# Kernel optimization log

Measured on AMD Instinct MI355X. Metric: run time of the kernel, lower is better.

## Reference

```python
import jax, jax.numpy as jnp
import numpy as np

N, C, H, DH = 4096, 256, 8, 32
E = 32768
MAX_SPD = 3
DEG_B = 8
LN_EPS = 1e-5


def _ln(h, g, b):
    mu = jnp.mean(h, axis=-1, keepdims=True)
    var = jnp.mean((h - mu) ** 2, axis=-1, keepdims=True)
    return g * (h - mu) / jnp.sqrt(var + LN_EPS) + b


def setup_inputs() -> dict:
    key = jax.random.key(0)
    ks = jax.random.split(key, 16)
    s = 1.0 / np.sqrt(C).astype(np.float32)
    s4 = 1.0 / np.sqrt(4 * C).astype(np.float32)
    return {
        "x": jax.random.normal(ks[0], (N, C), jnp.float32),
        "edge_index": jax.random.randint(ks[1], (2, E), 0, N, dtype=jnp.int32),
        "Wq": jax.random.normal(ks[2], (C, C), jnp.float32) * s,
        "bq": jnp.zeros((C,), jnp.float32),
        "Wk": jax.random.normal(ks[3], (C, C), jnp.float32) * s,
        "bk": jnp.zeros((C,), jnp.float32),
        "Wv": jax.random.normal(ks[4], (C, C), jnp.float32) * s,
        "bv": jnp.zeros((C,), jnp.float32),
        "Wo": jax.random.normal(ks[5], (C, C), jnp.float32) * s,
        "bo": jnp.zeros((C,), jnp.float32),
        "W1": jax.random.normal(ks[6], (C, 4 * C), jnp.float32) * s,
        "b1": jnp.zeros((4 * C,), jnp.float32),
        "W2": jax.random.normal(ks[7], (4 * C, C), jnp.float32) * s4,
        "b2": jnp.zeros((C,), jnp.float32),
        "g1": jnp.ones((C,), jnp.float32),
        "beta1": jnp.zeros((C,), jnp.float32),
        "g2": jnp.ones((C,), jnp.float32),
        "beta2": jnp.zeros((C,), jnp.float32),
        # spd_emb is zero-init in torch; use small random so the bias path is exercised
        "spd_emb": jax.random.normal(ks[8], (MAX_SPD + 2, H), jnp.float32) * 0.02,
        "in_deg_emb": jax.random.normal(ks[9], (DEG_B + 1, C), jnp.float32) * 0.02,
        "out_deg_emb": jax.random.normal(ks[10], (DEG_B + 1, C), jnp.float32) * 0.02,
        "et_bias": jax.random.normal(ks[11], (), jnp.float32) * 0.02,
    }


def _bucket(d):
    # floor(log2(d+1)) clamped to [0, DEG_B]
    return jnp.clip(jnp.floor(jnp.log2(d + 1.0)), 0, DEG_B).astype(jnp.int32)


def _spd_buckets(src, dst):
    # use_reverse_spd=True: adjacency A[row=dst, col=src]; anchors = dst, probe = src.
    # Frontier F starts as identity over all nodes (superset of unique-anchor columns;
    # extra columns never probed -> identical result to torch's unique-anchor version).
    F = jnp.eye(N, dtype=jnp.float32)
    spd = jnp.full((E,), MAX_SPD + 1, dtype=jnp.int32)
    unset = jnp.ones((E,), dtype=bool)
    for k in range(1, MAX_SPD + 1):
        # (A @ F) > 0  via edge-gather + per-row max (binary reachability)
        F = (jax.ops.segment_max(F[src], dst, num_segments=N) > 0).astype(jnp.float32)
        reach = F[src, dst] > 0  # probe anchor column dst at row src
        newly = unset & reach
        spd = jnp.where(newly, k, spd)
        unset = unset & ~newly
    return jnp.clip(spd, 1, MAX_SPD + 1)


def reference(x, edge_index, Wq, bq, Wk, bk, Wv, bv, Wo, bo, W1, b1, W2, b2,
              g1, beta1, g2, beta2, spd_emb, in_deg_emb, out_deg_emb, et_bias):
    src, dst = edge_index[0], edge_index[1]
    ones = jnp.ones((E,), jnp.float32)
    in_deg = jax.ops.segment_sum(ones, dst, num_segments=N)
    out_deg = jax.ops.segment_sum(ones, src, num_segments=N)
    x_in = x + in_deg_emb[_bucket(in_deg)] + out_deg_emb[_bucket(out_deg)]

    spd = _spd_buckets(src, dst)  # [E] int in [1, MAX_SPD+1]

    xn = _ln(x_in, g1, beta1)
    Q = (xn @ Wq + bq).reshape(N, H, DH)
    K = (xn @ Wk + bk).reshape(N, H, DH)
    V = (xn @ Wv + bv).reshape(N, H, DH)

    scores = jnp.sum(Q[dst] * K[src], axis=-1) / np.sqrt(DH)  # [E, H]
    scores = scores + spd_emb[spd] + et_bias

    # segment softmax over edges sharing a destination node
    m = jax.ops.segment_max(scores, dst, num_segments=N)  # [N, H]
    m = jnp.where(jnp.isfinite(m), m, 0.0)
    e = jnp.exp(scores - m[dst])
    ssum = jax.ops.segment_sum(e, dst, num_segments=N)
    w = e / jnp.where(ssum[dst] > 0, ssum[dst], 1.0)  # [E, H]

    msg = jax.ops.segment_sum(w[:, :, None] * V[src], dst, num_segments=N)  # [N,H,DH]
    h = x_in + msg.reshape(N, C) @ Wo + bo
    hn = _ln(h, g2, beta2)
    ff = jax.nn.gelu(hn @ W1 + b1, approximate=False) @ W2 + b2
    return h + ff
```

## Files before the change

kernel.cpp:

```cpp
#include <hip/hip_runtime.h>
#include <math.h>

#define NN 4096
#define CC 256
#define HH 8
#define DHD 32
#define EE 32768
#define FW 128
#define MAXD 128

typedef float f32x4 __attribute__((ext_vector_type(4)));
typedef __bf16 bf16x8 __attribute__((ext_vector_type(8)));
typedef __bf16 bf16x4 __attribute__((ext_vector_type(4)));

__device__ __forceinline__ int bucketf(int d){
  float l = log2f((float)d + 1.0f);
  int b = (int)floorf(l);
  return b < 0 ? 0 : (b > 8 ? 8 : b);
}

__global__ void k_deg(const int* __restrict__ src, const int* __restrict__ dst,
                      int* __restrict__ indeg, int* __restrict__ outdeg){
  int e = blockIdx.x*256 + threadIdx.x;
  if(e < EE){
    atomicAdd(&indeg[dst[e]], 1);
    atomicAdd(&outdeg[src[e]], 1);
  }
}

__global__ void k_scan(const int* __restrict__ deg, int* __restrict__ offs){
  __shared__ int part[1024];
  int t = threadIdx.x;
  int v0=deg[t*4], v1=deg[t*4+1], v2=deg[t*4+2], v3=deg[t*4+3];
  int s = v0+v1+v2+v3;
  part[t] = s;
  __syncthreads();
  for(int d=1; d<1024; d<<=1){
    int x = (t>=d) ? part[t-d] : 0;
    __syncthreads();
    part[t] += x;
    __syncthreads();
  }
  int base = (t>0) ? part[t-1] : 0;
  offs[t*4]   = base;
  offs[t*4+1] = base+v0;
  offs[t*4+2] = base+v0+v1;
  offs[t*4+3] = base+v0+v1+v2;
  if(t==1023) offs[4096] = base+s;
}

__global__ void k_scatter(const int* __restrict__ src, const int* __restrict__ dst,
                          const int* __restrict__ offs, int* __restrict__ cursor,
                          int* __restrict__ nsrc){
  int e = blockIdx.x*256+threadIdx.x;
  if(e<EE){
    int d = dst[e], s = src[e];
    int p = atomicAdd(&cursor[d],1);
    nsrc[offs[d]+p] = s;
  }
}

__global__ void k_mid(const int* __restrict__ offs, const int* __restrict__ nsrc,
                      unsigned* __restrict__ F1,
                      const float* __restrict__ x, const int* __restrict__ indeg,
                      const int* __restrict__ outdeg, const float* __restrict__ iemb,
                      const float* __restrict__ oemb, const float* __restrict__ g,
                      const float* __restrict__ be, float* __restrict__ x_in,
                      __bf16* __restrict__ xn){
  int b = blockIdx.x;
  int tid = threadIdx.x;
  if(b < 2048){
    int d = b*2 + (tid>>7);
    int w = tid & 127;
    int o0 = offs[d], o1 = offs[d+1];
    unsigned v = 0;
    for(int i=o0;i<o1;i++){
      int s = nsrc[i];
      if((s>>5) == w) v |= 1u << (s&31);
    }
    F1[(size_t)d*FW + w] = v;
    return;
  }
  int node = (b-2048)*4 + (tid >> 6);
  int lane = tid & 63;
  int bi = bucketf(indeg[node]);
  int bo = bucketf(outdeg[node]);
  float4 xv = ((const float4*)(x + (size_t)node*CC))[lane];
  float4 iv = ((const float4*)(iemb + (size_t)bi*CC))[lane];
  float4 ov = ((const float4*)(oemb + (size_t)bo*CC))[lane];
  float4 v;
  v.x = xv.x+iv.x+ov.x; v.y = xv.y+iv.y+ov.y;
  v.z = xv.z+iv.z+ov.z; v.w = xv.w+iv.w+ov.w;
  ((float4*)(x_in + (size_t)node*CC))[lane] = v;
  float s  = v.x+v.y+v.z+v.w;
  float sq = v.x*v.x+v.y*v.y+v.z*v.z+v.w*v.w;
  #pragma unroll
  for(int m=32;m>=1;m>>=1){ s += __shfl_xor(s,m); sq += __shfl_xor(sq,m); }
  float mu  = s * (1.0f/CC);
  float var = sq * (1.0f/CC) - mu*mu;
  float inv = rsqrtf(var + 1e-5f);
  float4 gv = ((const float4*)g)[lane];
  float4 bv = ((const float4*)be)[lane];
  bf16x4 o;
  o[0] = (__bf16)(gv.x*(v.x-mu)*inv + bv.x);
  o[1] = (__bf16)(gv.y*(v.y-mu)*inv + bv.y);
  o[2] = (__bf16)(gv.z*(v.z-mu)*inv + bv.z);
  o[3] = (__bf16)(gv.w*(v.w-mu)*inv + bv.w);
  *(bf16x4*)(xn + (size_t)node*CC + lane*4) = o;
}

__global__ void k_prop(const int* __restrict__ offs, const int* __restrict__ nsrc,
                       const unsigned* __restrict__ Fin, unsigned* __restrict__ Fout){
  int d = blockIdx.x; int w = threadIdx.x;
  int o0 = offs[d], o1 = offs[d+1];
  unsigned v = 0;
  for(int i=o0;i<o1;i++){
    int s = nsrc[i];
    v |= Fin[(size_t)s*FW + w];
  }
  Fout[(size_t)d*FW + w] = v;
}

__global__ void k_ln(const float* __restrict__ in, const float* __restrict__ g,
                     const float* __restrict__ b, __bf16* __restrict__ out){
  int node = blockIdx.x*4 + (threadIdx.x >> 6);
  int lane = threadIdx.x & 63;
  float4 v = ((const float4*)(in + (size_t)node*CC))[lane];
  float s  = v.x+v.y+v.z+v.w;
  float sq = v.x*v.x+v.y*v.y+v.z*v.z+v.w*v.w;
  #pragma unroll
  for(int m=32;m>=1;m>>=1){ s += __shfl_xor(s,m); sq += __shfl_xor(sq,m); }
  float mu  = s * (1.0f/CC);
  float var = sq * (1.0f/CC) - mu*mu;
  float inv = rsqrtf(var + 1e-5f);
  float4 gv = ((const float4*)g)[lane];
  float4 bv = ((const float4*)b)[lane];
  bf16x4 o;
  o[0] = (__bf16)(gv.x*(v.x-mu)*inv + bv.x);
  o[1] = (__bf16)(gv.y*(v.y-mu)*inv + bv.y);
  o[2] = (__bf16)(gv.z*(v.z-mu)*inv + bv.z);
  o[3] = (__bf16)(gv.w*(v.w-mu)*inv + bv.w);
  *(bf16x4*)(out + (size_t)node*CC + lane*4) = o;
}

__global__ void k_pre(const float* __restrict__ Wq, const float* __restrict__ Wk,
                      const float* __restrict__ Wv, const float* __restrict__ Wo,
                      const float* __restrict__ W1, const float* __restrict__ W2,
                      const float* __restrict__ bq, const float* __restrict__ bk,
                      const float* __restrict__ bv,
                      __bf16* __restrict__ WqkvT, __bf16* __restrict__ WoT,
                      __bf16* __restrict__ W1T, __bf16* __restrict__ W2T,
                      float* __restrict__ bqkv, int* __restrict__ zero_base){
  int b = blockIdx.x;
  int tid = threadIdx.x;
  if(b >= 193){
    zero_base[(b-193)*256 + tid] = 0;
    return;
  }
  if(b == 192){
    bqkv[tid]     = bq[tid];
    bqkv[256+tid] = bk[tid];
    bqkv[512+tid] = bv[tid];
    return;
  }
  const float* W; __bf16* Wt; int K, N, tile;
  if(b < 16)      { W=Wq; Wt=WqkvT;        K=256;  N=256;  tile=b; }
  else if(b < 32) { W=Wk; Wt=WqkvT+65536;  K=256;  N=256;  tile=b-16; }
  else if(b < 48) { W=Wv; Wt=WqkvT+131072; K=256;  N=256;  tile=b-32; }
  else if(b < 64) { W=Wo; Wt=WoT;          K=256;  N=256;  tile=b-48; }
  else if(b < 128){ W=W1; Wt=W1T;          K=256;  N=1024; tile=b-64; }
  else            { W=W2; Wt=W2T;          K=1024; N=256;  tile=b-128; }
  int nK = K/64;
  int tk = tile % nK, tn = tile / nK;
  __shared__ float T[64][65];
  int c = tid & 63, r0 = tid >> 6;
  #pragma unroll
  for(int i=0;i<16;i++){
    int row = r0*16 + i;
    T[row][c] = W[(size_t)(tk*64+row)*N + tn*64 + c];
  }
  __syncthreads();
  #pragma unroll
  for(int i=0;i<16;i++){
    int row = r0*16 + i;
    Wt[(size_t)(tn*64+row)*K + tk*64 + c] = (__bf16)T[c][row];
  }
}

template<int MODE>
__global__ __launch_bounds__(256) void k_bgemm(const __bf16* __restrict__ A, const __bf16* __restrict__ Bt,
                       const float* __restrict__ bias, const float* __restrict__ add,
                       float* __restrict__ outf, __bf16* __restrict__ outb,
                       int M, int N, int K){
  __shared__ __bf16 As[64*64];
  __shared__ __bf16 Bs[64*64];
  const int tid = threadIdx.x;
  const int lane = tid & 63, w = tid >> 6;
  const int wr = w >> 1, wc = w & 1;
  const int l15 = lane & 15, g = lane >> 4;
  const int bm = blockIdx.y*64, bn = blockIdx.x*64;
  f32x4 acc[2][2] = {};
  for(int k0=0; k0<K; k0+=64){
    #pragma unroll
    for(int rep=0; rep<2; rep++){
      int q = tid + rep*256;
      int row = q>>3;
      int scb = ((q&7)*16) ^ ((row&7)<<4);
      const __bf16* srcA = A  + (size_t)(bm+row)*K + k0 + (scb>>1);
      const __bf16* srcB = Bt + (size_t)(bn+row)*K + k0 + (scb>>1);
      __builtin_amdgcn_global_load_lds(
        (const __attribute__((address_space(1))) void*)srcA,
        (__attribute__((address_space(3))) void*)((char*)As + q*16), 16, 0, 0);
      __builtin_amdgcn_global_load_lds(
        (const __attribute__((address_space(1))) void*)srcB,
        (__attribute__((address_space(3))) void*)((char*)Bs + q*16), 16, 0, 0);
    }
    __syncthreads();
    #pragma unroll
    for(int ks=0; ks<2; ks++){
      bf16x8 a[2], b[2];
      #pragma unroll
      for(int i=0;i<2;i++){
        int row = wr*32 + i*16 + l15;
        int byte_ = row*128 + ks*64 + g*16; byte_ ^= (row&7)<<4;
        a[i] = *(const bf16x8*)((const char*)As + byte_);
      }
      #pragma unroll
      for(int j=0;j<2;j++){
        int row = wc*32 + j*16 + l15;
        int byte_ = row*128 + ks*64 + g*16; byte_ ^= (row&7)<<4;
        b[j] = *(const bf16x8*)((const char*)Bs + byte_);
      }
      #pragma unroll
      for(int i=0;i<2;i++)
        #pragma unroll
        for(int j=0;j<2;j++)
          acc[i][j] = __builtin_amdgcn_mfma_f32_16x16x32_bf16(a[i], b[j], acc[i][j], 0, 0, 0);
    }
    __syncthreads();
  }
  #pragma unroll
  for(int i=0;i<2;i++){
    #pragma unroll
    for(int j=0;j<2;j++){
      int col = bn + wc*32 + j*16 + l15;
      float bv = bias[col];
      #pragma unroll
      for(int r=0;r<4;r++){
        int rowg = bm + wr*32 + i*16 + g*4 + r;
        float v = acc[i][j][r] + bv;
        if(MODE==1) v += add[(size_t)rowg*N + col];
        if(MODE==2){
          v = 0.5f*v*(1.0f + erff(v*0.70710678118654752f));
          outb[(size_t)rowg*N + col] = (__bf16)v;
        } else if(MODE==3){
          outb[(size_t)rowg*N + col] = (__bf16)v;
        } else {
          outf[(size_t)rowg*N + col] = v;
        }
      }
    }
  }
}

__global__ void k_sagg(const int* __restrict__ nsrc, const int* __restrict__ offs,
                       const __bf16* __restrict__ QKV,
                       const unsigned* __restrict__ F1, const unsigned* __restrict__ F2,
                       const unsigned* __restrict__ F3,
                       const float* __restrict__ spde, __bf16* __restrict__ msg){
  __shared__ float scs[MAXD][9];
  __shared__ int   sl[MAXD];
  __shared__ int   spi[MAXD];
  const int d = blockIdx.x;
  const int t = threadIdx.x;
  const int o0 = offs[d];
  int deg = offs[d+1] - o0; if(deg > MAXD) deg = MAXD;
  if(t < deg){
    int s = nsrc[o0+t];
    sl[t] = s;
    size_t wi = (size_t)s*FW + (d>>5); unsigned bb = 1u << (d&31);
    int sp = 4;
    if(F3[wi] & bb) sp = 3;
    if(F2[wi] & bb) sp = 2;
    if(F1[wi] & bb) sp = 1;
    spi[t] = sp;
  }
  __syncthreads();
  { const int h = t & 7, i0 = t >> 3;
    const bf16x8* qr = (const bf16x8*)(QKV + (size_t)d*768 + h*DHD);
    for(int i=i0; i<deg; i+=32){
      const bf16x8* kr = (const bf16x8*)(QKV + (size_t)sl[i]*768 + 256 + h*DHD);
      float acc = 0.f;
      #pragma unroll
      for(int j=0;j<4;j++){
        bf16x8 kv = kr[j], qv = qr[j];
        #pragma unroll
        for(int u=0;u<8;u++) acc += (float)qv[u] * (float)kv[u];
      }
      scs[i][h] = acc * 0.17677669529663687f + spde[spi[i]*HH + h];
    }
  }
  __syncthreads();
  { const int h = t >> 5, l = t & 31;
    float m = -3.0e38f;
    for(int i=l;i<deg;i+=32) m = fmaxf(m, scs[i][h]);
    #pragma unroll
    for(int mk=16;mk>=1;mk>>=1) m = fmaxf(m, __shfl_xor(m,mk));
    float ss = 0.f;
    for(int i=l;i<deg;i+=32) ss += expf(scs[i][h]-m);
    #pragma unroll
    for(int mk=16;mk>=1;mk>>=1) ss += __shfl_xor(ss,mk);
    float inv = (ss>0.f) ? 1.f/ss : 1.f;
    for(int i=l;i<deg;i+=32) scs[i][h] = expf(scs[i][h]-m)*inv;
  }
  __syncthreads();
  { const int h = t >> 5, c = t & 31;
    float acc = 0.f;
    for(int i=0;i<deg;i++)
      acc += scs[i][h] * (float)QKV[(size_t)sl[i]*768 + 512 + h*DHD + c];
    msg[(size_t)d*CC + h*DHD + c] = (__bf16)acc;
  }
}

extern "C" void kernel_launch(void* const* d_in, const int* in_sizes, int n_in,
                              void* d_out, int out_size, void* d_ws, size_t ws_size,
                              hipStream_t stream){
  const float* x  = (const float*)d_in[0];
  const int*  ei  = (const int*)d_in[1];
  const float* Wq = (const float*)d_in[2];  const float* bq = (const float*)d_in[3];
  const float* Wk = (const float*)d_in[4];  const float* bk = (const float*)d_in[5];
  const float* Wv = (const float*)d_in[6];  const float* bv = (const float*)d_in[7];
  const float* Wo = (const float*)d_in[8];  const float* bo = (const float*)d_in[9];
  const float* W1 = (const float*)d_in[10]; const float* b1 = (const float*)d_in[11];
  const float* W2 = (const float*)d_in[12]; const float* b2 = (const float*)d_in[13];
  const float* g1 = (const float*)d_in[14]; const float* be1= (const float*)d_in[15];
  const float* g2 = (const float*)d_in[16]; const float* be2= (const float*)d_in[17];
  const float* spde = (const float*)d_in[18];
  const float* iemb = (const float*)d_in[19];
  const float* oemb = (const float*)d_in[20];
  const float* etb  = (const float*)d_in[21]; (void)etb;
  const int* src = ei;
  const int* dst = ei + EE;
  float* out = (float*)d_out;

  const size_t NC = (size_t)NN*CC;
  float* ws   = (float*)d_ws;
  float* x_in = ws;
  float* hbuf = ws + NC;
  int* indeg  = (int*)(ws + 2*NC);
  int* outdeg = indeg + NN;
  int* cursor = outdeg + NN;
  unsigned* F1 = (unsigned*)(cursor + NN);
  unsigned* F2 = F1 + (size_t)NN*FW;
  unsigned* F3 = F2 + (size_t)NN*FW;
  __bf16* QKV  = (__bf16*)(F3 + (size_t)NN*FW);
  __bf16* xn_bf  = (__bf16*)(ws + 5517312);
  __bf16* msg_bf = (__bf16*)(ws + 6041600);
  __bf16* WqkvT  = (__bf16*)(ws + 6565888);
  __bf16* WoT    = WqkvT + 196608;
  __bf16* W1T    = WoT + 65536;
  __bf16* W2T    = W1T + 262144;
  float* bqkv    = ws + 6959104;
  int* offs      = (int*)(bqkv + 768);
  int* nsrc      = offs + NN + 4;
  __bf16* ff1_bf = (__bf16*)(ws + 2*NC);
  __bf16* hn_bf  = (__bf16*)(ws + 4*NC);

  k_pre<<<241,256,0,stream>>>(Wq,Wk,Wv,Wo,W1,W2,bq,bk,bv,WqkvT,WoT,W1T,W2T,bqkv,indeg);
  k_deg<<<EE/256,256,0,stream>>>(src,dst,indeg,outdeg);
  k_scan<<<1,1024,0,stream>>>(indeg,offs);
  k_scatter<<<EE/256,256,0,stream>>>(src,dst,offs,cursor,nsrc);
  k_mid<<<3072,256,0,stream>>>(offs,nsrc,F1,x,indeg,outdeg,iemb,oemb,g1,be1,x_in,xn_bf);
  k_prop<<<NN,FW,0,stream>>>(offs,nsrc,F1,F2);
  k_prop<<<NN,FW,0,stream>>>(offs,nsrc,F2,F3);

  dim3 gq(768/64, NN/64);
  k_bgemm<3><<<gq,256,0,stream>>>(xn_bf, WqkvT, bqkv, nullptr, nullptr, QKV, NN, 768, 256);

  k_sagg<<<NN,256,0,stream>>>(nsrc,offs,QKV,F1,F2,F3,spde,msg_bf);

  dim3 go(256/64, NN/64);
  k_bgemm<1><<<go,256,0,stream>>>(msg_bf, WoT, bo, x_in, hbuf, nullptr, NN, 256, 256);
  k_ln <<<NN/4,256,0,stream>>>(hbuf,g2,be2,hn_bf);
  dim3 gf1(1024/64, NN/64);
  k_bgemm<2><<<gf1,256,0,stream>>>(hn_bf, W1T, b1, nullptr, nullptr, ff1_bf, NN, 1024, 256);
  dim3 gf2(256/64, NN/64);
  k_bgemm<1><<<gf2,256,0,stream>>>(ff1_bf, W2T, b2, hbuf, out, nullptr, NN, 256, 1024);
}
```

Before: 92.04 us.

## Replace CSR build with fixed-width adjacency and fuse third hop with QKV GEMM

Drops the degree-count and prefix-scan kernels by scattering sources straight into a fixed-stride per-node slot array (MAXD=64), with the atomic cursor reused as in-degree and out-degree counted in the scatter. The third frontier propagation is merged into the QKV projection GEMM as one launch with block-index branching, so the two independent jobs share the GPU. This cuts launches and serial single-block scan work. It truncates neighbors beyond 64 per node, which is only safe if no node exceeds that in-degree (MAXD was also lowered from 128 for the aggregation).

```diff
diff --git a/kernel.cpp b/kernel.cpp
--- a/kernel.cpp
+++ b/kernel.cpp
@@ -7,7 +7,7 @@
 #define DHD 32
 #define EE 32768
 #define FW 128
-#define MAXD 128
+#define MAXD 64
 
 typedef float f32x4 __attribute__((ext_vector_type(4)));
 typedef __bf16 bf16x8 __attribute__((ext_vector_type(8)));
@@ -19,50 +19,21 @@
   return b < 0 ? 0 : (b > 8 ? 8 : b);
 }
 
-__global__ void k_deg(const int* __restrict__ src, const int* __restrict__ dst,
-                      int* __restrict__ indeg, int* __restrict__ outdeg){
-  int e = blockIdx.x*256 + threadIdx.x;
-  if(e < EE){
-    atomicAdd(&indeg[dst[e]], 1);
-    atomicAdd(&outdeg[src[e]], 1);
-  }
-}
-
-__global__ void k_scan(const int* __restrict__ deg, int* __restrict__ offs){
-  __shared__ int part[1024];
-  int t = threadIdx.x;
-  int v0=deg[t*4], v1=deg[t*4+1], v2=deg[t*4+2], v3=deg[t*4+3];
-  int s = v0+v1+v2+v3;
-  part[t] = s;
-  __syncthreads();
-  for(int d=1; d<1024; d<<=1){
-    int x = (t>=d) ? part[t-d] : 0;
-    __syncthreads();
-    part[t] += x;
-    __syncthreads();
-  }
-  int base = (t>0) ? part[t-1] : 0;
-  offs[t*4]   = base;
-  offs[t*4+1] = base+v0;
-  offs[t*4+2] = base+v0+v1;
-  offs[t*4+3] = base+v0+v1+v2;
-  if(t==1023) offs[4096] = base+s;
-}
-
 __global__ void k_scatter(const int* __restrict__ src, const int* __restrict__ dst,
-                          const int* __restrict__ offs, int* __restrict__ cursor,
+                          int* __restrict__ cursor, int* __restrict__ outdeg,
                           int* __restrict__ nsrc){
   int e = blockIdx.x*256+threadIdx.x;
   if(e<EE){
     int d = dst[e], s = src[e];
+    atomicAdd(&outdeg[s],1);
     int p = atomicAdd(&cursor[d],1);
-    nsrc[offs[d]+p] = s;
-  }
-}
-
-__global__ void k_mid(const int* __restrict__ offs, const int* __restrict__ nsrc,
+    if(p < MAXD) nsrc[d*MAXD+p] = s;
+  }
+}
+
+__global__ void k_mid(const int* __restrict__ cursor, const int* __restrict__ nsrc,
                       unsigned* __restrict__ F1,
-                      const float* __restrict__ x, const int* __restrict__ indeg,
+                      const float* __restrict__ x,
                       const int* __restrict__ outdeg, const float* __restrict__ iemb,
                       const float* __restrict__ oemb, const float* __restrict__ g,
                       const float* __restrict__ be, float* __restrict__ x_in,
@@ -72,10 +43,11 @@
   if(b < 2048){
     int d = b*2 + (tid>>7);
     int w = tid & 127;
-    int o0 = offs[d], o1 = offs[d+1];
+    int cdeg = cursor[d]; if(cdeg > MAXD) cdeg = MAXD;
+    const int* row = nsrc + d*MAXD;
     unsigned v = 0;
-    for(int i=o0;i<o1;i++){
-      int s = nsrc[i];
+    for(int i=0;i<cdeg;i++){
+      int s = row[i];
       if((s>>5) == w) v |= 1u << (s&31);
     }
     F1[(size_t)d*FW + w] = v;
@@ -83,7 +55,7 @@
   }
   int node = (b-2048)*4 + (tid >> 6);
   int lane = tid & 63;
-  int bi = bucketf(indeg[node]);
+  int bi = bucketf(cursor[node]);
   int bo = bucketf(outdeg[node]);
   float4 xv = ((const float4*)(x + (size_t)node*CC))[lane];
   float4 iv = ((const float4*)(iemb + (size_t)bi*CC))[lane];
@@ -109,14 +81,14 @@
   *(bf16x4*)(xn + (size_t)node*CC + lane*4) = o;
 }
 
-__global__ void k_prop(const int* __restrict__ offs, const int* __restrict__ nsrc,
+__global__ void k_prop(const int* __restrict__ cursor, const int* __restrict__ nsrc,
                        const unsigned* __restrict__ Fin, unsigned* __restrict__ Fout){
   int d = blockIdx.x; int w = threadIdx.x;
-  int o0 = offs[d], o1 = offs[d+1];
+  int cdeg = cursor[d]; if(cdeg > MAXD) cdeg = MAXD;
+  const int* row = nsrc + d*MAXD;
   unsigned v = 0;
-  for(int i=o0;i<o1;i++){
-    int s = nsrc[i];
-    v |= Fin[(size_t)s*FW + w];
+  for(int i=0;i<cdeg;i++){
+    v |= Fin[(size_t)row[i]*FW + w];
   }
   Fout[(size_t)d*FW + w] = v;
 }
@@ -195,7 +167,8 @@
   __shared__ __bf16 As[64*64];
   __shared__ __bf16 Bs[64*64];
   const int tid = threadIdx.x;
-  const int lane = tid & 63, w = tid >> 6;
+  const int lane = tid & 63;
+  const int w = tid >> 6;
   const int wr = w >> 1, wc = w & 1;
   const int l15 = lane & 15, g = lane >> 4;
   const int bm = blockIdx.y*64, bn = blockIdx.x*64;
@@ -263,7 +236,87 @@
   }
 }
 
-__global__ void k_sagg(const int* __restrict__ nsrc, const int* __restrict__ offs,
+__global__ __launch_bounds__(256) void k_pq(const int* __restrict__ cursor, const int* __restrict__ nsrc,
+                    const unsigned* __restrict__ F2, unsigned* __restrict__ F3,
+                    const __bf16* __restrict__ A, const __bf16* __restrict__ Bt,
+                    const float* __restrict__ bias, __bf16* __restrict__ outb){
+  __shared__ __bf16 As[64*64];
+  __shared__ __bf16 Bs[64*64];
+  const int b = blockIdx.x;
+  const int tid = threadIdx.x;
+  if(b < 2048){
+    int d = b*2 + (tid>>7);
+    int w_ = tid & 127;
+    int cdeg = cursor[d]; if(cdeg > MAXD) cdeg = MAXD;
+    const int* row = nsrc + d*MAXD;
+    unsigned v = 0;
+    for(int i=0;i<cdeg;i++) v |= F2[(size_t)row[i]*FW + w_];
+    F3[(size_t)d*FW + w_] = v;
+    return;
+  }
+  const int bx = b - 2048;
+  const int N = 768, K = 256;
+  const int bm = (bx/12)*64, bn = (bx%12)*64;
+  const int lane = tid & 63;
+  const int w = tid >> 6;
+  const int wr = w >> 1, wc = w & 1;
+  const int l15 = lane & 15, g = lane >> 4;
+  f32x4 acc[2][2] = {};
+  for(int k0=0; k0<K; k0+=64){
+    #pragma unroll
+    for(int rep=0; rep<2; rep++){
+      int q = tid + rep*256;
+      int row = q>>3;
+      int scb = ((q&7)*16) ^ ((row&7)<<4);
+      const __bf16* srcA = A  + (size_t)(bm+row)*K + k0 + (scb>>1);
+      const __bf16* srcB = Bt + (size_t)(bn+row)*K + k0 + (scb>>1);
+      __builtin_amdgcn_global_load_lds(
+        (const __attribute__((address_space(1))) void*)srcA,
+        (__attribute__((address_space(3))) void*)((char*)As + q*16), 16, 0, 0);
+      __builtin_amdgcn_global_load_lds(
+        (const __attribute__((address_space(1))) void*)srcB,
+        (__attribute__((address_space(3))) void*)((char*)Bs + q*16), 16, 0, 0);
+    }
+    __syncthreads();
+    #pragma unroll
+    for(int ks=0; ks<2; ks++){
+      bf16x8 a[2], bb[2];
+      #pragma unroll
+      for(int i=0;i<2;i++){
+        int row = wr*32 + i*16 + l15;
+        int byte_ = row*128 + ks*64 + g*16; byte_ ^= (row&7)<<4;
+        a[i] = *(const bf16x8*)((const char*)As + byte_);
+      }
+      #pragma unroll
+      for(int j=0;j<2;j++){
+        int row = wc*32 + j*16 + l15;
+        int byte_ = row*128 + ks*64 + g*16; byte_ ^= (row&7)<<4;
+        bb[j] = *(const bf16x8*)((const char*)Bs + byte_);
+      }
+      #pragma unroll
+      for(int i=0;i<2;i++)
+        #pragma unroll
+        for(int j=0;j<2;j++)
+          acc[i][j] = __builtin_amdgcn_mfma_f32_16x16x32_bf16(a[i], bb[j], acc[i][j], 0, 0, 0);
+    }
+    __syncthreads();
+  }
+  #pragma unroll
+  for(int i=0;i<2;i++){
+    #pragma unroll
+    for(int j=0;j<2;j++){
+      int col = bn + wc*32 + j*16 + l15;
+      float bv = bias[col];
+      #pragma unroll
+      for(int r=0;r<4;r++){
+        int rowg = bm + wr*32 + i*16 + g*4 + r;
+        outb[(size_t)rowg*N + col] = (__bf16)(acc[i][j][r] + bv);
+      }
+    }
+  }
+}
+
+__global__ void k_sagg(const int* __restrict__ nsrc, const int* __restrict__ cursor,
                        const __bf16* __restrict__ QKV,
                        const unsigned* __restrict__ F1, const unsigned* __restrict__ F2,
                        const unsigned* __restrict__ F3,
@@ -273,10 +326,9 @@
   __shared__ int   spi[MAXD];
   const int d = blockIdx.x;
   const int t = threadIdx.x;
-  const int o0 = offs[d];
-  int deg = offs[d+1] - o0; if(deg > MAXD) deg = MAXD;
+  int deg = cursor[d]; if(deg > MAXD) deg = MAXD;
   if(t < deg){
-    int s = nsrc[o0+t];
+    int s = nsrc[d*MAXD+t];
     sl[t] = s;
     size_t wi = (size_t)s*FW + (d>>5); unsigned bb = 1u << (d&31);
     int sp = 4;
@@ -347,13 +399,13 @@
   float* ws   = (float*)d_ws;
   float* x_in = ws;
   float* hbuf = ws + NC;
-  int* indeg  = (int*)(ws + 2*NC);
-  int* outdeg = indeg + NN;
-  int* cursor = outdeg + NN;
-  unsigned* F1 = (unsigned*)(cursor + NN);
+  int* cursor = (int*)(ws + 2*NC);
+  int* outdeg = cursor + NN;
+  unsigned* F1 = (unsigned*)(ws + 2*NC + 12288);
   unsigned* F2 = F1 + (size_t)NN*FW;
   unsigned* F3 = F2 + (size_t)NN*FW;
   __bf16* QKV  = (__bf16*)(F3 + (size_t)NN*FW);
+  int* nsrc    = (int*)(ws + 5255168);
   __bf16* xn_bf  = (__bf16*)(ws + 5517312);
   __bf16* msg_bf = (__bf16*)(ws + 6041600);
   __bf16* WqkvT  = (__bf16*)(ws + 6565888);
@@ -361,24 +413,15 @@
   __bf16* W1T    = WoT + 65536;
   __bf16* W2T    = W1T + 262144;
   float* bqkv    = ws + 6959104;
-  int* offs      = (int*)(bqkv + 768);
-  int* nsrc      = offs + NN + 4;
   __bf16* ff1_bf = (__bf16*)(ws + 2*NC);
   __bf16* hn_bf  = (__bf16*)(ws + 4*NC);
 
-  k_pre<<<241,256,0,stream>>>(Wq,Wk,Wv,Wo,W1,W2,bq,bk,bv,WqkvT,WoT,W1T,W2T,bqkv,indeg);
-  k_deg<<<EE/256,256,0,stream>>>(src,dst,indeg,outdeg);
-  k_scan<<<1,1024,0,stream>>>(indeg,offs);
-  k_scatter<<<EE/256,256,0,stream>>>(src,dst,offs,cursor,nsrc);
-  k_mid<<<3072,256,0,stream>>>(offs,nsrc,F1,x,indeg,outdeg,iemb,oemb,g1,be1,x_in,xn_bf);
-  k_prop<<<NN,FW,0,stream>>>(offs,nsrc,F1,F2);
-  k_prop<<<NN,FW,0,stream>>>(offs,nsrc,F2,F3);
-
-  dim3 gq(768/64, NN/64);
-  k_bgemm<3><<<gq,256,0,stream>>>(xn_bf, WqkvT, bqkv, nullptr, nullptr, QKV, NN, 768, 256);
-
-  k_sagg<<<NN,256,0,stream>>>(nsrc,offs,QKV,F1,F2,F3,spde,msg_bf);
-
+  k_pre<<<225,256,0,stream>>>(Wq,Wk,Wv,Wo,W1,W2,bq,bk,bv,WqkvT,WoT,W1T,W2T,bqkv,cursor);
+  k_scatter<<<EE/256,256,0,stream>>>(src,dst,cursor,outdeg,nsrc);
+  k_mid<<<3072,256,0,stream>>>(cursor,nsrc,F1,x,outdeg,iemb,oemb,g1,be1,x_in,xn_bf);
+  k_prop<<<NN,FW,0,stream>>>(cursor,nsrc,F1,F2);
+  k_pq<<<2816,256,0,stream>>>(cursor,nsrc,F2,F3,xn_bf,WqkvT,bqkv,QKV);
+  k_sagg<<<NN,256,0,stream>>>(nsrc,cursor,QKV,F1,F2,F3,spde,msg_bf);
   dim3 go(256/64, NN/64);
   k_bgemm<1><<<go,256,0,stream>>>(msg_bf, WoT, bo, x_in, hbuf, nullptr, NN, 256, 256);
   k_ln <<<NN/4,256,0,stream>>>(hbuf,g2,be2,hn_bf);
```

After: 82.10 us. 10.8% less time.
